# Kernel tuning notes

Measured on AMD Instinct MI355X. Metric: run time of the kernel, lower is better.

The kernel has to match this reference:

```python
import jax, jax.numpy as jnp
import numpy as np

B, C, HEADS, W, Hh = 8, 512, 8, 32, 32
D = C // HEADS  # 64 per-head dim
N = W * Hh      # 1024 spatial tokens


def setup_inputs() -> dict:
    key = jax.random.key(0)
    ks = jax.random.split(key, 10)
    s = 1.0 / np.sqrt(C)
    return {
        "x": jax.random.normal(ks[0], (B, C, W, Hh), dtype=jnp.float32),
        "Wq": jax.random.normal(ks[1], (C, C), dtype=jnp.float32) * s,
        "bq": jax.random.normal(ks[2], (C,), dtype=jnp.float32) * 0.01,
        "Wk": jax.random.normal(ks[3], (C, C), dtype=jnp.float32) * s,
        "bk": jax.random.normal(ks[4], (C,), dtype=jnp.float32) * 0.01,
        "Wv": jax.random.normal(ks[5], (C, C), dtype=jnp.float32) * s,
        "bv": jax.random.normal(ks[6], (C,), dtype=jnp.float32) * 0.01,
        "rel_h": jax.random.normal(ks[7], (1, HEADS, D, 1, Hh), dtype=jnp.float32),
        "rel_w": jax.random.normal(ks[8], (1, HEADS, D, W, 1), dtype=jnp.float32),
    }


def reference(x, Wq, bq, Wk, bk, Wv, bv, rel_h, rel_w):
    b = x.shape[0]
    xf = x.reshape(b, C, N)  # [B, C, N] — 1x1 conv == per-position linear
    proj = lambda Wm, bm: (jnp.einsum('oc,bcn->bon', Wm, xf) + bm[None, :, None]).reshape(b, HEADS, D, N)
    q = proj(Wq, bq)  # [B, H, D, N]
    k = proj(Wk, bk)
    v = proj(Wv, bv)
    # content-content: q^T k -> [B, H, N, N]
    cc = jnp.einsum('bhdn,bhdm->bhnm', q, k)
    # relative position bias: (rel_h + rel_w) -> [H, D, N], then rel^T @ q
    rel = (rel_h + rel_w).reshape(HEADS, D, N)
    cp = jnp.einsum('hdn,bhdm->bhnm', rel, q)  # [B, H, N, N]
    attn = jax.nn.softmax(cc + cp, axis=-1)
    # out = v @ attn^T : out[d,m] = sum_n v[d,n] * attn[m,n]
    out = jnp.einsum('bhdn,bhmn->bhdm', v, attn)  # [B, H, D, N]
    return out.reshape(b, C, W, Hh)
```

## Files before the change

kernel.cpp:

```cpp
#include <hip/hip_runtime.h>

typedef _Float16 half8 __attribute__((ext_vector_type(8)));
typedef _Float16 half4 __attribute__((ext_vector_type(4)));
typedef float f32x4 __attribute__((ext_vector_type(4)));

__device__ __forceinline__ void glds16(const void* g, void* l) {
    __builtin_amdgcn_global_load_lds(
        (const __attribute__((address_space(1))) unsigned int*)g,
        (__attribute__((address_space(3))) unsigned int*)l, 16, 0, 0);
}


__global__ void k_prep_all(const float* __restrict__ Wq, const float* __restrict__ Wk,
                           const float* __restrict__ Wv, const float* __restrict__ bq,
                           const float* __restrict__ bk, const float* __restrict__ bv,
                           const float* __restrict__ x, const float* __restrict__ rel_h,
                           const float* __restrict__ rel_w, _Float16* __restrict__ Wf,
                           float* __restrict__ bias2, _Float16* __restrict__ xTf,
                           _Float16* __restrict__ rel2) {
    __shared__ float xs[64][65];
    int bid = blockIdx.x;
    if (bid < 384) {
        int t = bid * 256 + threadIdx.x;
        int m = t >> 6;
        int c8 = (t & 63) << 3;
        const float* src = (m < 512) ? (Wq + m * 512)
                         : (m < 1024 ? (Wk + (m - 512) * 512) : (Wv + (m - 1024) * 512));
        float4 v0 = *(const float4*)(src + c8);
        float4 v1 = *(const float4*)(src + c8 + 4);
        half8 o;
        o[0] = (_Float16)v0.x; o[1] = (_Float16)v0.y; o[2] = (_Float16)v0.z; o[3] = (_Float16)v0.w;
        o[4] = (_Float16)v1.x; o[5] = (_Float16)v1.y; o[6] = (_Float16)v1.z; o[7] = (_Float16)v1.w;
        *(half8*)(Wf + (size_t)m * 512 + c8) = o;
        if (t < 1536)
            bias2[t] = (t < 512) ? bq[t] : (t < 1024 ? bk[t - 512] : bv[t - 1024]);
    } else if (bid < 1408) {
        int i = bid - 384;
        int nt = (i & 15) << 6, ct = ((i >> 4) & 7) << 6, b = i >> 7;
        int t = threadIdx.x;
        const float* xb = x + ((size_t)b * 512 + ct) * 1024 + nt;
#pragma unroll
        for (int p = 0; p < 4; ++p) {
            int c = p * 16 + (t >> 4), n4 = (t & 15) * 4;
            float4 v = *(const float4*)(xb + (size_t)c * 1024 + n4);
            xs[c][n4] = v.x; xs[c][n4 + 1] = v.y; xs[c][n4 + 2] = v.z; xs[c][n4 + 3] = v.w;
        }
        __syncthreads();
        int nl = t >> 2, part = t & 3;
        _Float16* rowp = xTf + ((size_t)b * 1024 + nt + nl) * 512;
#pragma unroll
        for (int g = 0; g < 2; ++g) {
            half8 o;
#pragma unroll
            for (int j = 0; j < 8; ++j)
                o[j] = (_Float16)xs[part * 16 + g * 8 + j][nl];
            *(half8*)(rowp + ct + part * 16 + g * 8) = o;
        }
    } else {
        int tid = (bid - 1408) * 256 + threadIdx.x;
        int h = tid >> 13;
        int rem = tid & 8191;
        int n = rem >> 3;
        int g = rem & 7;
        int hh = n & 31, ww = n >> 5;
        half8 o;
#pragma unroll
        for (int j = 0; j < 8; ++j) {
            int d = g * 8 + j;
            o[j] = (_Float16)(rel_h[(h * 64 + d) * 32 + hh] + rel_w[(h * 64 + d) * 32 + ww]);
        }
        *(half8*)(rel2 + ((size_t)h * 1024 + n) * 64 + g * 8) = o;
    }
}

__global__ __launch_bounds__(256, 3) void k_proj(const _Float16* __restrict__ Wf,
                                                 const _Float16* __restrict__ xTf,
                                                 const float* __restrict__ bias2,
                                                 _Float16* __restrict__ q2,
                                                 _Float16* __restrict__ k2,
                                                 _Float16* __restrict__ vb) {
    __shared__ __align__(16) _Float16 As[8192];
    __shared__ __align__(16) _Float16 Bs[8192];
    int t = threadIdx.x;
    int lane = t & 63, w = t >> 6;
    int lm = lane & 15, lq = lane >> 4;
    int wr = (w >> 1) * 64, wc = (w & 1) * 64;
    int mb = blockIdx.y * 128, nb = blockIdx.x * 128, b = blockIdx.z;
    int rl = lane >> 2;
    int csw = ((lane & 3) ^ ((lane >> 3) & 3)) * 8;
    const _Float16* Ag0 = Wf + (size_t)(mb + w * 32 + rl) * 512 + csw;
    const _Float16* Ag1 = Ag0 + 16 * 512;
    const _Float16* Bg0 = xTf + ((size_t)b * 1024 + nb + w * 32 + rl) * 512 + csw;
    const _Float16* Bg1 = Bg0 + 16 * 512;
    f32x4 acc[4][4];
#pragma unroll
    for (int i = 0; i < 4; ++i)
#pragma unroll
        for (int j = 0; j < 4; ++j) acc[i][j] = {0.f, 0.f, 0.f, 0.f};
    int fsw = (lq ^ ((lm >> 1) & 3)) * 8;
    for (int k0 = 0; k0 < 512; k0 += 64) {
#pragma unroll
        for (int kh = 0; kh < 2; ++kh) {
            int ko = k0 + kh * 32;
            glds16(Ag0 + ko, &As[kh * 4096 + (w * 32) * 32]);
            glds16(Ag1 + ko, &As[kh * 4096 + (w * 32 + 16) * 32]);
            glds16(Bg0 + ko, &Bs[kh * 4096 + (w * 32) * 32]);
            glds16(Bg1 + ko, &Bs[kh * 4096 + (w * 32 + 16) * 32]);
        }
        __syncthreads();
#pragma unroll
        for (int kh = 0; kh < 2; ++kh) {
            half8 af[4], bfr[4];
#pragma unroll
            for (int mt = 0; mt < 4; ++mt)
                af[mt] = *(half8*)&As[kh * 4096 + (wr + mt * 16 + lm) * 32 + fsw];
#pragma unroll
            for (int nt = 0; nt < 4; ++nt)
                bfr[nt] = *(half8*)&Bs[kh * 4096 + (wc + nt * 16 + lm) * 32 + fsw];
#pragma unroll
            for (int mt = 0; mt < 4; ++mt)
#pragma unroll
                for (int nt = 0; nt < 4; ++nt)
                    acc[mt][nt] = __builtin_amdgcn_mfma_f32_16x16x32_f16(af[mt], bfr[nt], acc[mt][nt], 0, 0, 0);
        }
        __syncthreads();
    }
    int sect = mb >> 9;
    int hloc = ((mb & 511) + wr) >> 6;
    size_t bh = (size_t)b * 8 + hloc;
    if (sect < 2) {
        float sc = (sect == 0) ? 1.44269504089f : 1.0f;
        _Float16* dst = (sect == 0 ? q2 : k2) + bh * 1024 * 64;
#pragma unroll
        for (int mt = 0; mt < 4; ++mt) {
            int d0 = mt * 16 + lq * 4;
            float bi0 = bias2[mb + wr + d0];
            float bi1 = bias2[mb + wr + d0 + 1];
            float bi2 = bias2[mb + wr + d0 + 2];
            float bi3 = bias2[mb + wr + d0 + 3];
#pragma unroll
            for (int nt = 0; nt < 4; ++nt) {
                int n = nb + wc + nt * 16 + lm;
                half4 o;
                o[0] = (_Float16)((acc[mt][nt][0] + bi0) * sc);
                o[1] = (_Float16)((acc[mt][nt][1] + bi1) * sc);
                o[2] = (_Float16)((acc[mt][nt][2] + bi2) * sc);
                o[3] = (_Float16)((acc[mt][nt][3] + bi3) * sc);
                *(half4*)(dst + (size_t)n * 64 + d0) = o;
            }
        }
    } else {
        _Float16* dst = vb + bh * 64 * 1024;
#pragma unroll
        for (int mt = 0; mt < 4; ++mt)
#pragma unroll
            for (int reg = 0; reg < 4; ++reg) {
                int d = mt * 16 + lq * 4 + reg;
                float bi = bias2[mb + wr + d];
#pragma unroll
                for (int nt = 0; nt < 4; ++nt) {
                    int n = nb + wc + nt * 16 + lm;
                    dst[(size_t)d * 1024 + n] = (_Float16)(acc[mt][nt][reg] + bi);
                }
            }
    }
}

__global__ __launch_bounds__(256, 3) void k_attn(const _Float16* __restrict__ q2,
                                                 const _Float16* __restrict__ k2,
                                                 const _Float16* __restrict__ rel2,
                                                 const _Float16* __restrict__ vb,
                                                 float* __restrict__ out) {
    __shared__ __align__(16) char pool[45056];
    _Float16* kb_s = (_Float16*)pool;
    _Float16* v_s  = (_Float16*)(pool + 17408);
    _Float16* p_s  = (_Float16*)(pool + 26624);
    int t = threadIdx.x;
    int lane = t & 63, w = t >> 6;
    int lm = lane & 15, lq = lane >> 4;
    int lin = blockIdx.x;
    int mt0 = lin >> 6;
    int bh_ = lin & 63;
    int h = bh_ & 7, b = bh_ >> 3;
    size_t bh = (size_t)b * 8 + h;
    const _Float16* q2b = q2 + bh * 1024 * 64;
    const _Float16* k2b = k2 + bh * 1024 * 64;
    const _Float16* relb = rel2 + (size_t)h * 1024 * 64;
    const _Float16* vbb = vb + bh * 64 * 1024;
    float* outb = out + bh * 64 * 1024 + mt0 * 128;

    int r = t >> 2, part = t & 3;
    const _Float16* ksrc = ((part < 2) ? (k2b + part * 32) : (q2b + (part - 2) * 32));
    int vc = (t & 3) * 16;
    const _Float16* vsrcb = vbb + (size_t)r * 1024 + vc;
    _Float16* kdst = kb_s + r * 136 + part * 32;
    _Float16* vdst = v_s + r * 72 + vc;

    uint4 kc0, kc1, kc2, kc3, vv0, vv1;
    {
        const uint4* s_ = (const uint4*)(ksrc + (size_t)r * 64);
        kc0 = s_[0]; kc1 = s_[1]; kc2 = s_[2]; kc3 = s_[3];
        const uint4* v_ = (const uint4*)vsrcb;
        vv0 = v_[0]; vv1 = v_[1];
    }

    {
        int n = mt0 * 128 + r;
        const _Float16* src = (part < 2) ? (q2b + (size_t)n * 64 + part * 32)
                                         : (relb + (size_t)n * 64 + (part - 2) * 32);
        ((uint4*)kdst)[0] = ((const uint4*)src)[0];
        ((uint4*)kdst)[1] = ((const uint4*)src)[1];
        ((uint4*)kdst)[2] = ((const uint4*)src)[2];
        ((uint4*)kdst)[3] = ((const uint4*)src)[3];
    }
    __syncthreads();
    half8 ah0[4], ah1[4];
#pragma unroll
    for (int kk = 0; kk < 4; ++kk)
        ah0[kk] = *(half8*)&kb_s[(w * 16 + lm) * 136 + kk * 32 + lq * 8];
    __syncthreads();
    {
        int n = mt0 * 128 + 64 + r;
        const _Float16* src = (part < 2) ? (q2b + (size_t)n * 64 + part * 32)
                                         : (relb + (size_t)n * 64 + (part - 2) * 32);
        ((uint4*)kdst)[0] = ((const uint4*)src)[0];
        ((uint4*)kdst)[1] = ((const uint4*)src)[1];
        ((uint4*)kdst)[2] = ((const uint4*)src)[2];
        ((uint4*)kdst)[3] = ((const uint4*)src)[3];
    }
    __syncthreads();
#pragma unroll
    for (int kk = 0; kk < 4; ++kk)
        ah1[kk] = *(half8*)&kb_s[(w * 16 + lm) * 136 + kk * 32 + lq * 8];
    __syncthreads();

    f32x4 acco0[4], acco1[4];
#pragma unroll
    for (int i = 0; i < 4; ++i) { acco0[i] = {0.f, 0.f, 0.f, 0.f}; acco1[i] = {0.f, 0.f, 0.f, 0.f}; }
    float mrun0 = -3e38f, lrun0 = 0.f, mrun1 = -3e38f, lrun1 = 0.f;

    for (int kt = 0; kt < 16; ++kt) {
        ((uint4*)kdst)[0] = kc0;
        ((uint4*)kdst)[1] = kc1;
        ((uint4*)kdst)[2] = kc2;
        ((uint4*)kdst)[3] = kc3;
        ((uint4*)vdst)[0] = vv0;
        ((uint4*)vdst)[1] = vv1;
        __syncthreads();
        int nn = ((kt + 1) & 15) * 64;
        const uint4* s_ = (const uint4*)(ksrc + (size_t)(nn + r) * 64);
        uint4 kn0 = s_[0], kn1 = s_[1], kn2 = s_[2], kn3 = s_[3];
        const uint4* v_ = (const uint4*)(vsrcb + nn);
        uint4 vn0 = v_[0], vn1 = v_[1];
        f32x4 s0[4], s1[4];
#pragma unroll
        for (int ct = 0; ct < 4; ++ct) { s0[ct] = {0.f, 0.f, 0.f, 0.f}; s1[ct] = {0.f, 0.f, 0.f, 0.f}; }
#pragma unroll
        for (int ct = 0; ct < 4; ++ct) {
            half8 kf[4];
#pragma unroll
            for (int kk = 0; kk < 4; ++kk)
                kf[kk] = *(half8*)&kb_s[(ct * 16 + lm) * 136 + kk * 32 + lq * 8];
#pragma unroll
            for (int kk = 0; kk < 4; ++kk) {
                s0[ct] = __builtin_amdgcn_mfma_f32_16x16x32_f16(kf[kk], ah0[kk], s0[ct], 0, 0, 0);
                s1[ct] = __builtin_amdgcn_mfma_f32_16x16x32_f16(kf[kk], ah1[kk], s1[ct], 0, 0, 0);
            }
        }
        {
            float mx = -3e38f;
#pragma unroll
            for (int ct = 0; ct < 4; ++ct)
#pragma unroll
                for (int reg = 0; reg < 4; ++reg) mx = fmaxf(mx, s0[ct][reg]);
            mx = fmaxf(mx, __shfl_xor(mx, 16));
            mx = fmaxf(mx, __shfl_xor(mx, 32));
            float mnew = fmaxf(mrun0, mx);
            float al_ = exp2f(mrun0 - mnew);
            float rs = 0.f;
#pragma unroll
            for (int ct = 0; ct < 4; ++ct) {
                float p0 = exp2f(s0[ct][0] - mnew);
                float p1 = exp2f(s0[ct][1] - mnew);
                float p2 = exp2f(s0[ct][2] - mnew);
                float p3 = exp2f(s0[ct][3] - mnew);
                rs += (p0 + p1) + (p2 + p3);
                half4 o; o[0] = (_Float16)p0; o[1] = (_Float16)p1; o[2] = (_Float16)p2; o[3] = (_Float16)p3;
                *(half4*)&p_s[(w * 16 + lm) * 72 + ct * 16 + lq * 4] = o;
            }
            rs += __shfl_xor(rs, 16);
            rs += __shfl_xor(rs, 32);
            lrun0 = lrun0 * al_ + rs;
            mrun0 = mnew;
#pragma unroll
            for (int dt = 0; dt < 4; ++dt) {
                acco0[dt][0] *= al_; acco0[dt][1] *= al_;
                acco0[dt][2] *= al_; acco0[dt][3] *= al_;
            }
        }
        {
            float mx = -3e38f;
#pragma unroll
            for (int ct = 0; ct < 4; ++ct)
#pragma unroll
                for (int reg = 0; reg < 4; ++reg) mx = fmaxf(mx, s1[ct][reg]);
            mx = fmaxf(mx, __shfl_xor(mx, 16));
            mx = fmaxf(mx, __shfl_xor(mx, 32));
            float mnew = fmaxf(mrun1, mx);
            float al_ = exp2f(mrun1 - mnew);
            float rs = 0.f;
#pragma unroll
            for (int ct = 0; ct < 4; ++ct) {
                float p0 = exp2f(s1[ct][0] - mnew);
                float p1 = exp2f(s1[ct][1] - mnew);
                float p2 = exp2f(s1[ct][2] - mnew);
                float p3 = exp2f(s1[ct][3] - mnew);
                rs += (p0 + p1) + (p2 + p3);
                half4 o; o[0] = (_Float16)p0; o[1] = (_Float16)p1; o[2] = (_Float16)p2; o[3] = (_Float16)p3;
                *(half4*)&p_s[(64 + w * 16 + lm) * 72 + ct * 16 + lq * 4] = o;
            }
            rs += __shfl_xor(rs, 16);
            rs += __shfl_xor(rs, 32);
            lrun1 = lrun1 * al_ + rs;
            mrun1 = mnew;
#pragma unroll
            for (int dt = 0; dt < 4; ++dt) {
                acco1[dt][0] *= al_; acco1[dt][1] *= al_;
                acco1[dt][2] *= al_; acco1[dt][3] *= al_;
            }
        }
        half8 p0f[2], p1f[2];
#pragma unroll
        for (int ch = 0; ch < 2; ++ch) {
            p0f[ch] = *(half8*)&p_s[(w * 16 + lm) * 72 + ch * 32 + lq * 8];
            p1f[ch] = *(half8*)&p_s[(64 + w * 16 + lm) * 72 + ch * 32 + lq * 8];
        }
#pragma unroll
        for (int dt = 0; dt < 4; ++dt) {
            half8 vf0 = *(half8*)&v_s[(dt * 16 + lm) * 72 + lq * 8];
            half8 vf1 = *(half8*)&v_s[(dt * 16 + lm) * 72 + 32 + lq * 8];
            acco0[dt] = __builtin_amdgcn_mfma_f32_16x16x32_f16(vf0, p0f[0], acco0[dt], 0, 0, 0);
            acco0[dt] = __builtin_amdgcn_mfma_f32_16x16x32_f16(vf1, p0f[1], acco0[dt], 0, 0, 0);
            acco1[dt] = __builtin_amdgcn_mfma_f32_16x16x32_f16(vf0, p1f[0], acco1[dt], 0, 0, 0);
            acco1[dt] = __builtin_amdgcn_mfma_f32_16x16x32_f16(vf1, p1f[1], acco1[dt], 0, 0, 0);
        }
        __syncthreads();
        kc0 = kn0; kc1 = kn1; kc2 = kn2; kc3 = kn3;
        vv0 = vn0; vv1 = vn1;
    }
    float li0 = 1.f / lrun0, li1 = 1.f / lrun1;
#pragma unroll
    for (int dt = 0; dt < 4; ++dt)
#pragma unroll
        for (int reg = 0; reg < 4; ++reg) {
            int d = dt * 16 + lq * 4 + reg;
            outb[(size_t)d * 1024 + w * 16 + lm] = acco0[dt][reg] * li0;
            outb[(size_t)d * 1024 + 64 + w * 16 + lm] = acco1[dt][reg] * li1;
        }
}

extern "C" void kernel_launch(void* const* d_in, const int* in_sizes, int n_in,
                              void* d_out, int out_size, void* d_ws, size_t ws_size,
                              hipStream_t stream) {
    const float* x     = (const float*)d_in[0];
    const float* Wq    = (const float*)d_in[1];
    const float* bq    = (const float*)d_in[2];
    const float* Wk    = (const float*)d_in[3];
    const float* bk    = (const float*)d_in[4];
    const float* Wv    = (const float*)d_in[5];
    const float* bv    = (const float*)d_in[6];
    const float* rel_h = (const float*)d_in[7];
    const float* rel_w = (const float*)d_in[8];
    char* ws = (char*)d_ws;
    _Float16* Wf   = (_Float16*)(ws);
    float* bias2   = (float*)(ws + 1572864);
    _Float16* xTf  = (_Float16*)(ws + 1579008);
    _Float16* q2   = (_Float16*)(ws + 9967616);
    _Float16* k2   = (_Float16*)(ws + 18356224);
    _Float16* vb   = (_Float16*)(ws + 26744832);
    _Float16* rel2 = (_Float16*)(ws + 35133440);
    float* out = (float*)d_out;

    hipLaunchKernelGGL(k_prep_all, dim3(1664),     dim3(256), 0, stream,
                       Wq, Wk, Wv, bq, bk, bv, x, rel_h, rel_w, Wf, bias2, xTf, rel2);
    hipLaunchKernelGGL(k_proj,     dim3(8, 12, 8), dim3(256), 0, stream, Wf, xTf, bias2, q2, k2, vb);
    hipLaunchKernelGGL(k_attn,     dim3(512),      dim3(256), 0, stream, q2, k2, rel2, vb, out);
}
```

Baseline: 153.6 us.

## Halve attention query tile, double grid, add lazy rescale and MFMA priority

The attention kernel now processes 64 query rows per block instead of 128, doubling the grid to 1024 blocks. This shrinks shared memory and registers, so launch bounds go from 3 to 4 blocks per CU for more parallelism. It also rescales the running max only when it grows by more than 8, packs probabilities with cvt_pkrtz, and raises wave priority around the MFMA sections. The trade-off is that each K/V tile is reloaded twice as often per query row, and the skipped rescaling and round-toward-zero conversion slightly change numerics.

```diff
diff --git a/kernel.cpp b/kernel.cpp
--- a/kernel.cpp
+++ b/kernel.cpp
@@ -2,6 +2,7 @@
 
 typedef _Float16 half8 __attribute__((ext_vector_type(8)));
 typedef _Float16 half4 __attribute__((ext_vector_type(4)));
+typedef __fp16 fp16x2 __attribute__((ext_vector_type(2)));
 typedef float f32x4 __attribute__((ext_vector_type(4)));
 
 __device__ __forceinline__ void glds16(const void* g, void* l) {
@@ -166,12 +167,12 @@
     }
 }
 
-__global__ __launch_bounds__(256, 3) void k_attn(const _Float16* __restrict__ q2,
+__global__ __launch_bounds__(256, 4) void k_attn(const _Float16* __restrict__ q2,
                                                  const _Float16* __restrict__ k2,
                                                  const _Float16* __restrict__ rel2,
                                                  const _Float16* __restrict__ vb,
                                                  float* __restrict__ out) {
-    __shared__ __align__(16) char pool[45056];
+    __shared__ __align__(16) char pool[35840];
     _Float16* kb_s = (_Float16*)pool;
     _Float16* v_s  = (_Float16*)(pool + 17408);
     _Float16* p_s  = (_Float16*)(pool + 26624);
@@ -187,7 +188,7 @@
     const _Float16* k2b = k2 + bh * 1024 * 64;
     const _Float16* relb = rel2 + (size_t)h * 1024 * 64;
     const _Float16* vbb = vb + bh * 64 * 1024;
-    float* outb = out + bh * 64 * 1024 + mt0 * 128;
+    float* outb = out + bh * 64 * 1024 + mt0 * 64;
 
     int r = t >> 2, part = t & 3;
     const _Float16* ksrc = ((part < 2) ? (k2b + part * 32) : (q2b + (part - 2) * 32));
@@ -205,7 +206,7 @@
     }
 
     {
-        int n = mt0 * 128 + r;
+        int n = mt0 * 64 + r;
         const _Float16* src = (part < 2) ? (q2b + (size_t)n * 64 + part * 32)
                                          : (relb + (size_t)n * 64 + (part - 2) * 32);
         ((uint4*)kdst)[0] = ((const uint4*)src)[0];
@@ -214,30 +215,16 @@
         ((uint4*)kdst)[3] = ((const uint4*)src)[3];
     }
     __syncthreads();
-    half8 ah0[4], ah1[4];
+    half8 ah0[4];
 #pragma unroll
     for (int kk = 0; kk < 4; ++kk)
         ah0[kk] = *(half8*)&kb_s[(w * 16 + lm) * 136 + kk * 32 + lq * 8];
     __syncthreads();
-    {
-        int n = mt0 * 128 + 64 + r;
-        const _Float16* src = (part < 2) ? (q2b + (size_t)n * 64 + part * 32)
-                                         : (relb + (size_t)n * 64 + (part - 2) * 32);
-        ((uint4*)kdst)[0] = ((const uint4*)src)[0];
-        ((uint4*)kdst)[1] = ((const uint4*)src)[1];
-        ((uint4*)kdst)[2] = ((const uint4*)src)[2];
-        ((uint4*)kdst)[3] = ((const uint4*)src)[3];
-    }
-    __syncthreads();
-#pragma unroll
-    for (int kk = 0; kk < 4; ++kk)
-        ah1[kk] = *(half8*)&kb_s[(w * 16 + lm) * 136 + kk * 32 + lq * 8];
-    __syncthreads();
-
-    f32x4 acco0[4], acco1[4];
-#pragma unroll
-    for (int i = 0; i < 4; ++i) { acco0[i] = {0.f, 0.f, 0.f, 0.f}; acco1[i] = {0.f, 0.f, 0.f, 0.f}; }
-    float mrun0 = -3e38f, lrun0 = 0.f, mrun1 = -3e38f, lrun1 = 0.f;
+
+    f32x4 acco0[4];
+#pragma unroll
+    for (int i = 0; i < 4; ++i) acco0[i] = {0.f, 0.f, 0.f, 0.f};
+    float mrun0 = -3e38f, lrun0 = 0.f;
 
     for (int kt = 0; kt < 16; ++kt) {
         ((uint4*)kdst)[0] = kc0;
@@ -252,9 +239,10 @@
         uint4 kn0 = s_[0], kn1 = s_[1], kn2 = s_[2], kn3 = s_[3];
         const uint4* v_ = (const uint4*)(vsrcb + nn);
         uint4 vn0 = v_[0], vn1 = v_[1];
-        f32x4 s0[4], s1[4];
-#pragma unroll
-        for (int ct = 0; ct < 4; ++ct) { s0[ct] = {0.f, 0.f, 0.f, 0.f}; s1[ct] = {0.f, 0.f, 0.f, 0.f}; }
+        f32x4 s0[4];
+#pragma unroll
+        for (int ct = 0; ct < 4; ++ct) s0[ct] = {0.f, 0.f, 0.f, 0.f};
+        __builtin_amdgcn_s_setprio(1);
 #pragma unroll
         for (int ct = 0; ct < 4; ++ct) {
             half8 kf[4];
@@ -262,100 +250,74 @@
             for (int kk = 0; kk < 4; ++kk)
                 kf[kk] = *(half8*)&kb_s[(ct * 16 + lm) * 136 + kk * 32 + lq * 8];
 #pragma unroll
-            for (int kk = 0; kk < 4; ++kk) {
+            for (int kk = 0; kk < 4; ++kk)
                 s0[ct] = __builtin_amdgcn_mfma_f32_16x16x32_f16(kf[kk], ah0[kk], s0[ct], 0, 0, 0);
-                s1[ct] = __builtin_amdgcn_mfma_f32_16x16x32_f16(kf[kk], ah1[kk], s1[ct], 0, 0, 0);
-            }
-        }
+        }
+        __builtin_amdgcn_s_setprio(0);
         {
             float mx = -3e38f;
 #pragma unroll
-            for (int ct = 0; ct < 4; ++ct)
-#pragma unroll
-                for (int reg = 0; reg < 4; ++reg) mx = fmaxf(mx, s0[ct][reg]);
+            for (int ct = 0; ct < 4; ++ct) {
+                float a_ = fmaxf(s0[ct][0], s0[ct][1]);
+                float b2 = fmaxf(s0[ct][2], s0[ct][3]);
+                mx = fmaxf(mx, fmaxf(a_, b2));
+            }
             mx = fmaxf(mx, __shfl_xor(mx, 16));
             mx = fmaxf(mx, __shfl_xor(mx, 32));
-            float mnew = fmaxf(mrun0, mx);
-            float al_ = exp2f(mrun0 - mnew);
+            if (__any(mx > mrun0 + 8.f)) {
+                float mnew = fmaxf(mrun0, mx);
+                float al_ = exp2f(mrun0 - mnew);
+                lrun0 *= al_;
+#pragma unroll
+                for (int dt = 0; dt < 4; ++dt) {
+                    acco0[dt][0] *= al_; acco0[dt][1] *= al_;
+                    acco0[dt][2] *= al_; acco0[dt][3] *= al_;
+                }
+                mrun0 = mnew;
+            }
             float rs = 0.f;
 #pragma unroll
             for (int ct = 0; ct < 4; ++ct) {
-                float p0 = exp2f(s0[ct][0] - mnew);
-                float p1 = exp2f(s0[ct][1] - mnew);
-                float p2 = exp2f(s0[ct][2] - mnew);
-                float p3 = exp2f(s0[ct][3] - mnew);
+                float p0 = exp2f(s0[ct][0] - mrun0);
+                float p1 = exp2f(s0[ct][1] - mrun0);
+                float p2 = exp2f(s0[ct][2] - mrun0);
+                float p3 = exp2f(s0[ct][3] - mrun0);
                 rs += (p0 + p1) + (p2 + p3);
-                half4 o; o[0] = (_Float16)p0; o[1] = (_Float16)p1; o[2] = (_Float16)p2; o[3] = (_Float16)p3;
-                *(half4*)&p_s[(w * 16 + lm) * 72 + ct * 16 + lq * 4] = o;
+                fp16x2 lo = __builtin_amdgcn_cvt_pkrtz(p0, p1);
+                fp16x2 hi = __builtin_amdgcn_cvt_pkrtz(p2, p3);
+                uint2 pk;
+                pk.x = __builtin_bit_cast(unsigned int, lo);
+                pk.y = __builtin_bit_cast(unsigned int, hi);
+                *(uint2*)&p_s[(w * 16 + lm) * 72 + ct * 16 + lq * 4] = pk;
             }
             rs += __shfl_xor(rs, 16);
             rs += __shfl_xor(rs, 32);
-            lrun0 = lrun0 * al_ + rs;
-            mrun0 = mnew;
-#pragma unroll
-            for (int dt = 0; dt < 4; ++dt) {
-                acco0[dt][0] *= al_; acco0[dt][1] *= al_;
-                acco0[dt][2] *= al_; acco0[dt][3] *= al_;
-            }
-        }
-        {
-            float mx = -3e38f;
-#pragma unroll
-            for (int ct = 0; ct < 4; ++ct)
-#pragma unroll
-                for (int reg = 0; reg < 4; ++reg) mx = fmaxf(mx, s1[ct][reg]);
-            mx = fmaxf(mx, __shfl_xor(mx, 16));
-            mx = fmaxf(mx, __shfl_xor(mx, 32));
-            float mnew = fmaxf(mrun1, mx);
-            float al_ = exp2f(mrun1 - mnew);
-            float rs = 0.f;
-#pragma unroll
-            for (int ct = 0; ct < 4; ++ct) {
-                float p0 = exp2f(s1[ct][0] - mnew);
-                float p1 = exp2f(s1[ct][1] - mnew);
-                float p2 = exp2f(s1[ct][2] - mnew);
-                float p3 = exp2f(s1[ct][3] - mnew);
-                rs += (p0 + p1) + (p2 + p3);
-                half4 o; o[0] = (_Float16)p0; o[1] = (_Float16)p1; o[2] = (_Float16)p2; o[3] = (_Float16)p3;
-                *(half4*)&p_s[(64 + w * 16 + lm) * 72 + ct * 16 + lq * 4] = o;
-            }
-            rs += __shfl_xor(rs, 16);
-            rs += __shfl_xor(rs, 32);
-            lrun1 = lrun1 * al_ + rs;
-            mrun1 = mnew;
-#pragma unroll
-            for (int dt = 0; dt < 4; ++dt) {
-                acco1[dt][0] *= al_; acco1[dt][1] *= al_;
-                acco1[dt][2] *= al_; acco1[dt][3] *= al_;
-            }
-        }
-        half8 p0f[2], p1f[2];
-#pragma unroll
-        for (int ch = 0; ch < 2; ++ch) {
+            lrun0 += rs;
+        }
+        half8 p0f[2];
+#pragma unroll
+        for (int ch = 0; ch < 2; ++ch)
             p0f[ch] = *(half8*)&p_s[(w * 16 + lm) * 72 + ch * 32 + lq * 8];
-            p1f[ch] = *(half8*)&p_s[(64 + w * 16 + lm) * 72 + ch * 32 + lq * 8];
-        }
+        __builtin_amdgcn_s_setprio(1);
 #pragma unroll
         for (int dt = 0; dt < 4; ++dt) {
             half8 vf0 = *(half8*)&v_s[(dt * 16 + lm) * 72 + lq * 8];
             half8 vf1 = *(half8*)&v_s[(dt * 16 + lm) * 72 + 32 + lq * 8];
             acco0[dt] = __builtin_amdgcn_mfma_f32_16x16x32_f16(vf0, p0f[0], acco0[dt], 0, 0, 0);
             acco0[dt] = __builtin_amdgcn_mfma_f32_16x16x32_f16(vf1, p0f[1], acco0[dt], 0, 0, 0);
-            acco1[dt] = __builtin_amdgcn_mfma_f32_16x16x32_f16(vf0, p1f[0], acco1[dt], 0, 0, 0);
-            acco1[dt] = __builtin_amdgcn_mfma_f32_16x16x32_f16(vf1, p1f[1], acco1[dt], 0, 0, 0);
-        }
+        }
+        __builtin_amdgcn_s_setprio(0);
         __syncthreads();
         kc0 = kn0; kc1 = kn1; kc2 = kn2; kc3 = kn3;
         vv0 = vn0; vv1 = vn1;
     }
-    float li0 = 1.f / lrun0, li1 = 1.f / lrun1;
+    float li0 = 1.f / lrun0;
 #pragma unroll
     for (int dt = 0; dt < 4; ++dt)
 #pragma unroll
         for (int reg = 0; reg < 4; ++reg) {
             int d = dt * 16 + lq * 4 + reg;
             outb[(size_t)d * 1024 + w * 16 + lm] = acco0[dt][reg] * li0;
-            outb[(size_t)d * 1024 + 64 + w * 16 + lm] = acco1[dt][reg] * li1;
         }
 }
 
@@ -384,5 +346,5 @@
     hipLaunchKernelGGL(k_prep_all, dim3(1664),     dim3(256), 0, stream,
                        Wq, Wk, Wv, bq, bk, bv, x, rel_h, rel_w, Wf, bias2, xTf, rel2);
     hipLaunchKernelGGL(k_proj,     dim3(8, 12, 8), dim3(256), 0, stream, Wf, xTf, bias2, q2, k2, vb);
-    hipLaunchKernelGGL(k_attn,     dim3(512),      dim3(256), 0, stream, q2, k2, rel2, vb, out);
-}
+    hipLaunchKernelGGL(k_attn,     dim3(1024),     dim3(256), 0, stream, q2, k2, rel2, vb, out);
+}
```

Result: no change. 154.6 us (+0.6%).

## Double-buffer K/V tiles in LDS for attention kernel

Applied to the files above, without the earlier changes.

Splits the shared-memory K and V staging areas into two buffers, so the next tile is written to one buffer while the current tile is read from the other. This removes one barrier per key-tile iteration, and global prefetch now runs two tiles ahead. The Q and rel prologue loads into two buffers at once instead of two sequential passes. The cost is more LDS (70 KB instead of 44 KB) and launch bounds lowered from 3 to 2 blocks per CU, which reduces occupancy. The loop still keeps a barrier at its end for the p_s reuse.

```diff
diff --git a/kernel.cpp b/kernel.cpp
--- a/kernel.cpp
+++ b/kernel.cpp
@@ -166,15 +166,17 @@
     }
 }
 
-__global__ __launch_bounds__(256, 3) void k_attn(const _Float16* __restrict__ q2,
+__global__ __launch_bounds__(256, 2) void k_attn(const _Float16* __restrict__ q2,
                                                  const _Float16* __restrict__ k2,
                                                  const _Float16* __restrict__ rel2,
                                                  const _Float16* __restrict__ vb,
                                                  float* __restrict__ out) {
-    __shared__ __align__(16) char pool[45056];
-    _Float16* kb_s = (_Float16*)pool;
-    _Float16* v_s  = (_Float16*)(pool + 17408);
-    _Float16* p_s  = (_Float16*)(pool + 26624);
+    __shared__ __align__(16) char pool[71680];
+    _Float16* kb0 = (_Float16*)pool;
+    _Float16* kb1 = (_Float16*)(pool + 17408);
+    _Float16* v0  = (_Float16*)(pool + 34816);
+    _Float16* v1  = (_Float16*)(pool + 44032);
+    _Float16* p_s = (_Float16*)(pool + 53248);
     int t = threadIdx.x;
     int lane = t & 63, w = t >> 6;
     int lm = lane & 15, lq = lane >> 4;
@@ -193,8 +195,8 @@
     const _Float16* ksrc = ((part < 2) ? (k2b + part * 32) : (q2b + (part - 2) * 32));
     int vc = (t & 3) * 16;
     const _Float16* vsrcb = vbb + (size_t)r * 1024 + vc;
-    _Float16* kdst = kb_s + r * 136 + part * 32;
-    _Float16* vdst = v_s + r * 72 + vc;
+    int kdo = r * 136 + part * 32;
+    int vdo = r * 72 + vc;
 
     uint4 kc0, kc1, kc2, kc3, vv0, vv1;
     {
@@ -206,32 +208,40 @@
 
     {
         int n = mt0 * 128 + r;
-        const _Float16* src = (part < 2) ? (q2b + (size_t)n * 64 + part * 32)
-                                         : (relb + (size_t)n * 64 + (part - 2) * 32);
-        ((uint4*)kdst)[0] = ((const uint4*)src)[0];
-        ((uint4*)kdst)[1] = ((const uint4*)src)[1];
-        ((uint4*)kdst)[2] = ((const uint4*)src)[2];
-        ((uint4*)kdst)[3] = ((const uint4*)src)[3];
+        const _Float16* srcA = (part < 2) ? (q2b + (size_t)n * 64 + part * 32)
+                                          : (relb + (size_t)n * 64 + (part - 2) * 32);
+        uint4* d0 = (uint4*)(kb0 + kdo);
+        d0[0] = ((const uint4*)srcA)[0];
+        d0[1] = ((const uint4*)srcA)[1];
+        d0[2] = ((const uint4*)srcA)[2];
+        d0[3] = ((const uint4*)srcA)[3];
+        const _Float16* srcB = (part < 2) ? (q2b + (size_t)(n + 64) * 64 + part * 32)
+                                          : (relb + (size_t)(n + 64) * 64 + (part - 2) * 32);
+        uint4* d1 = (uint4*)(kb1 + kdo);
+        d1[0] = ((const uint4*)srcB)[0];
+        d1[1] = ((const uint4*)srcB)[1];
+        d1[2] = ((const uint4*)srcB)[2];
+        d1[3] = ((const uint4*)srcB)[3];
     }
     __syncthreads();
     half8 ah0[4], ah1[4];
 #pragma unroll
-    for (int kk = 0; kk < 4; ++kk)
-        ah0[kk] = *(half8*)&kb_s[(w * 16 + lm) * 136 + kk * 32 + lq * 8];
+    for (int kk = 0; kk < 4; ++kk) {
+        ah0[kk] = *(half8*)&kb0[(w * 16 + lm) * 136 + kk * 32 + lq * 8];
+        ah1[kk] = *(half8*)&kb1[(w * 16 + lm) * 136 + kk * 32 + lq * 8];
+    }
     __syncthreads();
+
     {
-        int n = mt0 * 128 + 64 + r;
-        const _Float16* src = (part < 2) ? (q2b + (size_t)n * 64 + part * 32)
-                                         : (relb + (size_t)n * 64 + (part - 2) * 32);
-        ((uint4*)kdst)[0] = ((const uint4*)src)[0];
-        ((uint4*)kdst)[1] = ((const uint4*)src)[1];
-        ((uint4*)kdst)[2] = ((const uint4*)src)[2];
-        ((uint4*)kdst)[3] = ((const uint4*)src)[3];
-    }
-    __syncthreads();
-#pragma unroll
-    for (int kk = 0; kk < 4; ++kk)
-        ah1[kk] = *(half8*)&kb_s[(w * 16 + lm) * 136 + kk * 32 + lq * 8];
+        uint4* kd = (uint4*)(kb0 + kdo);
+        kd[0] = kc0; kd[1] = kc1; kd[2] = kc2; kd[3] = kc3;
+        uint4* vd = (uint4*)(v0 + vdo);
+        vd[0] = vv0; vd[1] = vv1;
+        const uint4* s_ = (const uint4*)(ksrc + (size_t)(64 + r) * 64);
+        kc0 = s_[0]; kc1 = s_[1]; kc2 = s_[2]; kc3 = s_[3];
+        const uint4* v_ = (const uint4*)(vsrcb + 64);
+        vv0 = v_[0]; vv1 = v_[1];
+    }
     __syncthreads();
 
     f32x4 acco0[4], acco1[4];
@@ -240,18 +250,21 @@
     float mrun0 = -3e38f, lrun0 = 0.f, mrun1 = -3e38f, lrun1 = 0.f;
 
     for (int kt = 0; kt < 16; ++kt) {
-        ((uint4*)kdst)[0] = kc0;
-        ((uint4*)kdst)[1] = kc1;
-        ((uint4*)kdst)[2] = kc2;
-        ((uint4*)kdst)[3] = kc3;
-        ((uint4*)vdst)[0] = vv0;
-        ((uint4*)vdst)[1] = vv1;
-        __syncthreads();
-        int nn = ((kt + 1) & 15) * 64;
+        _Float16* bwK = (kt & 1) ? kb0 : kb1;
+        _Float16* bwV = (kt & 1) ? v0 : v1;
+        {
+            uint4* kd = (uint4*)(bwK + kdo);
+            kd[0] = kc0; kd[1] = kc1; kd[2] = kc2; kd[3] = kc3;
+            uint4* vd = (uint4*)(bwV + vdo);
+            vd[0] = vv0; vd[1] = vv1;
+        }
+        int nn = ((kt + 2) & 15) * 64;
         const uint4* s_ = (const uint4*)(ksrc + (size_t)(nn + r) * 64);
         uint4 kn0 = s_[0], kn1 = s_[1], kn2 = s_[2], kn3 = s_[3];
         const uint4* v_ = (const uint4*)(vsrcb + nn);
         uint4 vn0 = v_[0], vn1 = v_[1];
+        const _Float16* brK = (kt & 1) ? kb1 : kb0;
+        const _Float16* brV = (kt & 1) ? v1 : v0;
         f32x4 s0[4], s1[4];
 #pragma unroll
         for (int ct = 0; ct < 4; ++ct) { s0[ct] = {0.f, 0.f, 0.f, 0.f}; s1[ct] = {0.f, 0.f, 0.f, 0.f}; }
@@ -260,7 +273,7 @@
             half8 kf[4];
 #pragma unroll
             for (int kk = 0; kk < 4; ++kk)
-                kf[kk] = *(half8*)&kb_s[(ct * 16 + lm) * 136 + kk * 32 + lq * 8];
+                kf[kk] = *(half8*)&brK[(ct * 16 + lm) * 136 + kk * 32 + lq * 8];
 #pragma unroll
             for (int kk = 0; kk < 4; ++kk) {
                 s0[ct] = __builtin_amdgcn_mfma_f32_16x16x32_f16(kf[kk], ah0[kk], s0[ct], 0, 0, 0);
@@ -337,8 +350,8 @@
         }
 #pragma unroll
         for (int dt = 0; dt < 4; ++dt) {
-            half8 vf0 = *(half8*)&v_s[(dt * 16 + lm) * 72 + lq * 8];
-            half8 vf1 = *(half8*)&v_s[(dt * 16 + lm) * 72 + 32 + lq * 8];
+            half8 vf0 = *(half8*)&brV[(dt * 16 + lm) * 72 + lq * 8];
+            half8 vf1 = *(half8*)&brV[(dt * 16 + lm) * 72 + 32 + lq * 8];
             acco0[dt] = __builtin_amdgcn_mfma_f32_16x16x32_f16(vf0, p0f[0], acco0[dt], 0, 0, 0);
             acco0[dt] = __builtin_amdgcn_mfma_f32_16x16x32_f16(vf1, p0f[1], acco0[dt], 0, 0, 0);
             acco1[dt] = __builtin_amdgcn_mfma_f32_16x16x32_f16(vf0, p1f[0], acco1[dt], 0, 0, 0);
```

Result: no change. 153.8 us (+0.1%).

## Load attention K/Q/V fragments directly from global, dropping LDS staging and barriers

Applied to the files above, without the earlier changes.

The attention kernel no longer stages K, Q and V tiles through shared memory with register double-buffering. Each wave now reads its MFMA fragments straight from global memory, and only the probability tile stays in LDS. This removes the per-iteration __syncthreads and the LDS store/load traffic, and the occupancy hint drops from 3 to 2 blocks per SM. In exchange, the four waves read the same K/V tiles redundantly through the cache with narrow strided accesses and no explicit prefetch. The projection kernel also swaps the batch and column-tile grid axes to change block scheduling order.

```diff
diff --git a/kernel.cpp b/kernel.cpp
--- a/kernel.cpp
+++ b/kernel.cpp
@@ -85,7 +85,7 @@
     int lane = t & 63, w = t >> 6;
     int lm = lane & 15, lq = lane >> 4;
     int wr = (w >> 1) * 64, wc = (w & 1) * 64;
-    int mb = blockIdx.y * 128, nb = blockIdx.x * 128, b = blockIdx.z;
+    int mb = blockIdx.y * 128, nb = blockIdx.z * 128, b = blockIdx.x;
     int rl = lane >> 2;
     int csw = ((lane & 3) ^ ((lane >> 3) & 3)) * 8;
     const _Float16* Ag0 = Wf + (size_t)(mb + w * 32 + rl) * 512 + csw;
@@ -166,15 +166,12 @@
     }
 }
 
-__global__ __launch_bounds__(256, 3) void k_attn(const _Float16* __restrict__ q2,
+__global__ __launch_bounds__(256, 2) void k_attn(const _Float16* __restrict__ q2,
                                                  const _Float16* __restrict__ k2,
                                                  const _Float16* __restrict__ rel2,
                                                  const _Float16* __restrict__ vb,
                                                  float* __restrict__ out) {
-    __shared__ __align__(16) char pool[45056];
-    _Float16* kb_s = (_Float16*)pool;
-    _Float16* v_s  = (_Float16*)(pool + 17408);
-    _Float16* p_s  = (_Float16*)(pool + 26624);
+    __shared__ __align__(16) _Float16 p_s[128 * 72];
     int t = threadIdx.x;
     int lane = t & 63, w = t >> 6;
     int lm = lane & 15, lq = lane >> 4;
@@ -189,50 +186,19 @@
     const _Float16* vbb = vb + bh * 64 * 1024;
     float* outb = out + bh * 64 * 1024 + mt0 * 128;
 
-    int r = t >> 2, part = t & 3;
-    const _Float16* ksrc = ((part < 2) ? (k2b + part * 32) : (q2b + (part - 2) * 32));
-    int vc = (t & 3) * 16;
-    const _Float16* vsrcb = vbb + (size_t)r * 1024 + vc;
-    _Float16* kdst = kb_s + r * 136 + part * 32;
-    _Float16* vdst = v_s + r * 72 + vc;
-
-    uint4 kc0, kc1, kc2, kc3, vv0, vv1;
+    half8 ah0[4], ah1[4];
     {
-        const uint4* s_ = (const uint4*)(ksrc + (size_t)r * 64);
-        kc0 = s_[0]; kc1 = s_[1]; kc2 = s_[2]; kc3 = s_[3];
-        const uint4* v_ = (const uint4*)vsrcb;
-        vv0 = v_[0]; vv1 = v_[1];
-    }
-
-    {
-        int n = mt0 * 128 + r;
-        const _Float16* src = (part < 2) ? (q2b + (size_t)n * 64 + part * 32)
-                                         : (relb + (size_t)n * 64 + (part - 2) * 32);
-        ((uint4*)kdst)[0] = ((const uint4*)src)[0];
-        ((uint4*)kdst)[1] = ((const uint4*)src)[1];
-        ((uint4*)kdst)[2] = ((const uint4*)src)[2];
-        ((uint4*)kdst)[3] = ((const uint4*)src)[3];
-    }
-    __syncthreads();
-    half8 ah0[4], ah1[4];
-#pragma unroll
-    for (int kk = 0; kk < 4; ++kk)
-        ah0[kk] = *(half8*)&kb_s[(w * 16 + lm) * 136 + kk * 32 + lq * 8];
-    __syncthreads();
-    {
-        int n = mt0 * 128 + 64 + r;
-        const _Float16* src = (part < 2) ? (q2b + (size_t)n * 64 + part * 32)
-                                         : (relb + (size_t)n * 64 + (part - 2) * 32);
-        ((uint4*)kdst)[0] = ((const uint4*)src)[0];
-        ((uint4*)kdst)[1] = ((const uint4*)src)[1];
-        ((uint4*)kdst)[2] = ((const uint4*)src)[2];
-        ((uint4*)kdst)[3] = ((const uint4*)src)[3];
-    }
-    __syncthreads();
-#pragma unroll
-    for (int kk = 0; kk < 4; ++kk)
-        ah1[kk] = *(half8*)&kb_s[(w * 16 + lm) * 136 + kk * 32 + lq * 8];
-    __syncthreads();
+        int n0 = mt0 * 128 + w * 16 + lm;
+#pragma unroll
+        for (int kk = 0; kk < 4; ++kk) {
+            const _Float16* s0p = (kk < 2) ? (q2b + (size_t)n0 * 64 + kk * 32 + lq * 8)
+                                           : (relb + (size_t)n0 * 64 + (kk - 2) * 32 + lq * 8);
+            ah0[kk] = *(const half8*)s0p;
+            const _Float16* s1p = (kk < 2) ? (q2b + (size_t)(n0 + 64) * 64 + kk * 32 + lq * 8)
+                                           : (relb + (size_t)(n0 + 64) * 64 + (kk - 2) * 32 + lq * 8);
+            ah1[kk] = *(const half8*)s1p;
+        }
+    }
 
     f32x4 acco0[4], acco1[4];
 #pragma unroll
@@ -240,32 +206,29 @@
     float mrun0 = -3e38f, lrun0 = 0.f, mrun1 = -3e38f, lrun1 = 0.f;
 
     for (int kt = 0; kt < 16; ++kt) {
-        ((uint4*)kdst)[0] = kc0;
-        ((uint4*)kdst)[1] = kc1;
-        ((uint4*)kdst)[2] = kc2;
-        ((uint4*)kdst)[3] = kc3;
-        ((uint4*)vdst)[0] = vv0;
-        ((uint4*)vdst)[1] = vv1;
-        __syncthreads();
-        int nn = ((kt + 1) & 15) * 64;
-        const uint4* s_ = (const uint4*)(ksrc + (size_t)(nn + r) * 64);
-        uint4 kn0 = s_[0], kn1 = s_[1], kn2 = s_[2], kn3 = s_[3];
-        const uint4* v_ = (const uint4*)(vsrcb + nn);
-        uint4 vn0 = v_[0], vn1 = v_[1];
+        int nn = kt * 64;
         f32x4 s0[4], s1[4];
 #pragma unroll
         for (int ct = 0; ct < 4; ++ct) { s0[ct] = {0.f, 0.f, 0.f, 0.f}; s1[ct] = {0.f, 0.f, 0.f, 0.f}; }
 #pragma unroll
         for (int ct = 0; ct < 4; ++ct) {
+            int nr = nn + ct * 16 + lm;
             half8 kf[4];
-#pragma unroll
-            for (int kk = 0; kk < 4; ++kk)
-                kf[kk] = *(half8*)&kb_s[(ct * 16 + lm) * 136 + kk * 32 + lq * 8];
+            kf[0] = *(const half8*)(k2b + (size_t)nr * 64 + lq * 8);
+            kf[1] = *(const half8*)(k2b + (size_t)nr * 64 + 32 + lq * 8);
+            kf[2] = *(const half8*)(q2b + (size_t)nr * 64 + lq * 8);
+            kf[3] = *(const half8*)(q2b + (size_t)nr * 64 + 32 + lq * 8);
 #pragma unroll
             for (int kk = 0; kk < 4; ++kk) {
                 s0[ct] = __builtin_amdgcn_mfma_f32_16x16x32_f16(kf[kk], ah0[kk], s0[ct], 0, 0, 0);
                 s1[ct] = __builtin_amdgcn_mfma_f32_16x16x32_f16(kf[kk], ah1[kk], s1[ct], 0, 0, 0);
             }
+        }
+        half8 vf0[4], vf1[4];
+#pragma unroll
+        for (int dt = 0; dt < 4; ++dt) {
+            vf0[dt] = *(const half8*)(vbb + (size_t)(dt * 16 + lm) * 1024 + nn + lq * 8);
+            vf1[dt] = *(const half8*)(vbb + (size_t)(dt * 16 + lm) * 1024 + nn + 32 + lq * 8);
         }
         {
             float mx = -3e38f;
@@ -337,16 +300,11 @@
         }
 #pragma unroll
         for (int dt = 0; dt < 4; ++dt) {
-            half8 vf0 = *(half8*)&v_s[(dt * 16 + lm) * 72 + lq * 8];
-            half8 vf1 = *(half8*)&v_s[(dt * 16 + lm) * 72 + 32 + lq * 8];
-            acco0[dt] = __builtin_amdgcn_mfma_f32_16x16x32_f16(vf0, p0f[0], acco0[dt], 0, 0, 0);
-            acco0[dt] = __builtin_amdgcn_mfma_f32_16x16x32_f16(vf1, p0f[1], acco0[dt], 0, 0, 0);
-            acco1[dt] = __builtin_amdgcn_mfma_f32_16x16x32_f16(vf0, p1f[0], acco1[dt], 0, 0, 0);
-            acco1[dt] = __builtin_amdgcn_mfma_f32_16x16x32_f16(vf1, p1f[1], acco1[dt], 0, 0, 0);
-        }
-        __syncthreads();
-        kc0 = kn0; kc1 = kn1; kc2 = kn2; kc3 = kn3;
-        vv0 = vn0; vv1 = vn1;
+            acco0[dt] = __builtin_amdgcn_mfma_f32_16x16x32_f16(vf0[dt], p0f[0], acco0[dt], 0, 0, 0);
+            acco0[dt] = __builtin_amdgcn_mfma_f32_16x16x32_f16(vf1[dt], p0f[1], acco0[dt], 0, 0, 0);
+            acco1[dt] = __builtin_amdgcn_mfma_f32_16x16x32_f16(vf0[dt], p1f[0], acco1[dt], 0, 0, 0);
+            acco1[dt] = __builtin_amdgcn_mfma_f32_16x16x32_f16(vf1[dt], p1f[1], acco1[dt], 0, 0, 0);
+        }
     }
     float li0 = 1.f / lrun0, li1 = 1.f / lrun1;
 #pragma unroll
```

After: 203.6 us. 1.32x slower.
